# Kernel optimization log

Measured on AMD Instinct MI355X. Metric: run time of the kernel, lower is better.

## Reference

```python
import jax, jax.numpy as jnp
import numpy as np

H = 16  # num_heads

def setup_inputs() -> dict:
    key = jax.random.key(0)
    k1, k2, k3 = jax.random.split(key, 3)
    D = 1024
    x = jax.random.normal(k1, (4, 2048, D), dtype=jnp.float32)
    W_qkv = jax.random.normal(k2, (D, 3 * D), dtype=jnp.float32) * (1.0 / np.sqrt(D))
    b_qkv = jnp.zeros((3 * D,), dtype=jnp.float32)
    W_out = jax.random.normal(k3, (D, D), dtype=jnp.float32) * (1.0 / np.sqrt(D))
    b_out = jnp.zeros((D,), dtype=jnp.float32)
    return {"x": x, "W_qkv": W_qkv, "b_qkv": b_qkv, "W_out": W_out, "b_out": b_out}

def reference(x, W_qkv, b_qkv, W_out, b_out):
    B, S, D = x.shape
    hd = D // H  # head_dim
    qkv = x @ W_qkv + b_qkv  # [B,S,3D]
    q, k, v = jnp.split(qkv, 3, axis=-1)
    # [B,S,D] -> [B,H,S,hd]
    q = q.reshape(B, S, H, hd).transpose(0, 2, 1, 3)
    k = k.reshape(B, S, H, hd).transpose(0, 2, 1, 3)
    v = v.reshape(B, S, H, hd).transpose(0, 2, 1, 3)
    scores = jnp.einsum('bhqd,bhkd->bhqk', q, k) / jnp.sqrt(jnp.float32(hd))
    weights = jax.nn.softmax(scores, axis=-1)  # dropout p=0.0 (eval)
    out = jnp.einsum('bhqk,bhkd->bhqd', weights, v)
    out = out.transpose(0, 2, 1, 3).reshape(B, S, D)
    return out @ W_out + b_out
```

## Files before the change

### kernel.cpp

```cpp
#include <hip/hip_runtime.h>

typedef __bf16 bf16;
typedef __bf16 bf16x4 __attribute__((ext_vector_type(4)));
typedef __bf16 bf16x8 __attribute__((ext_vector_type(8)));
typedef short s16x4 __attribute__((ext_vector_type(4)));
typedef float f32x4 __attribute__((ext_vector_type(4)));

static constexpr int NB = 4;
static constexpr int NS = 2048;
static constexpr int ND = 1024;
static constexpr int NH = 16;
static constexpr int HD = 64;
static constexpr float QSCALE = 0.18033688011112042f;

#define GL16(g, l)                                                             \
    __builtin_amdgcn_global_load_lds(                                          \
        (const __attribute__((address_space(1))) void*)(g),                    \
        (__attribute__((address_space(3))) void*)(l), 16, 0, 0)

static __device__ __forceinline__ unsigned pk2(float a, float b) {
    union { __bf16 h[2]; unsigned u; } t;
    t.h[0] = (__bf16)a; t.h[1] = (__bf16)b;
    return t.u;
}

__global__ void k_conv(const float* __restrict__ in, bf16* __restrict__ out, int n) {
    int i = (blockIdx.x * blockDim.x + threadIdx.x) * 4;
    if (i < n) {
        float4 v = *reinterpret_cast<const float4*>(in + i);
        bf16* o = out + i;
        o[0] = (bf16)v.x; o[1] = (bf16)v.y; o[2] = (bf16)v.z; o[3] = (bf16)v.w;
    }
}

__global__ void k_transconv(const float* __restrict__ in, bf16* __restrict__ out,
                            int K, int N) {
    __shared__ float tile[64][33];
    int k0 = blockIdx.y * 64, n0 = blockIdx.x * 32;
    int tx = threadIdx.x, ty = threadIdx.y;
#pragma unroll
    for (int i = 0; i < 8; ++i)
        tile[ty + 8 * i][tx] = in[(long)(k0 + ty + 8 * i) * N + n0 + tx];
    __syncthreads();
    int t = ty * 32 + tx;
    int row = t >> 3;
    int col8 = (t & 7) * 8;
    bf16x8 v;
#pragma unroll
    for (int c = 0; c < 8; ++c) v[c] = (bf16)tile[col8 + c][row];
    *reinterpret_cast<bf16x8*>(&out[(long)(n0 + row) * K + k0 + col8]) = v;
}

template <int MODE>
__global__ __launch_bounds__(256, 2) void k_gemm(
    const bf16* __restrict__ A, const bf16* __restrict__ Bt,
    const float* __restrict__ bias,
    void* __restrict__ out0, void* __restrict__ out1,
    int M, int Kd)
{
    constexpr int BM = 128, BN = 128, BK = 64;
    __shared__ __align__(16) bf16 As[2][BM * BK];
    __shared__ __align__(16) bf16 Bs[2][BN * BK];

    const int t = threadIdx.x;
    const int wid = t >> 6, lane = t & 63;
    const int wm = wid >> 1, wn = wid & 1;
    const int m0 = blockIdx.y * BM, n0 = blockIdx.x * BN;
    const int lrow = lane & 15, lhi = lane >> 4;

    const int srow0 = wid * 32 + (lane >> 3);
    const int scol = ((lane & 7) ^ (lane >> 3)) * 8;
    const bf16* ag = A + (long)(m0 + srow0) * Kd + scol;
    const bf16* bg = Bt + (long)(n0 + srow0) * Kd + scol;

    auto STAGE = [&](int buf_, int k0_) {
#pragma unroll
        for (int c = 0; c < 4; ++c) {
            GL16(ag + (long)(c * 8) * Kd + k0_, &As[buf_][(wid * 32 + c * 8) * BK]);
            GL16(bg + (long)(c * 8) * Kd + k0_, &Bs[buf_][(wid * 32 + c * 8) * BK]);
        }
    };

    f32x4 acc[4][4] = {};
    const int nt = Kd >> 6;
    const int swzr = (lrow & 7) << 4;
    int co[2];
#pragma unroll
    for (int kk = 0; kk < 2; ++kk)
        co[kk] = ((kk * 64 + lhi * 16) ^ swzr) >> 1;

    STAGE(0, 0);
    int cur = 0;
    for (int tix = 0; tix < nt; ++tix) {
        if (tix + 1 < nt) {
            STAGE(cur ^ 1, (tix + 1) * BK);
            asm volatile("s_waitcnt vmcnt(8)" ::: "memory");
        } else {
            asm volatile("s_waitcnt vmcnt(0)" ::: "memory");
        }
        __builtin_amdgcn_s_barrier();
        __builtin_amdgcn_sched_barrier(0);

        bf16x8 af[2][4], bfr[2][4];
#pragma unroll
        for (int kk = 0; kk < 2; ++kk)
#pragma unroll
            for (int i = 0; i < 4; ++i) {
                af[kk][i]  = *reinterpret_cast<const bf16x8*>(
                    &As[cur][(wm * 64 + i * 16 + lrow) * BK + co[kk]]);
                bfr[kk][i] = *reinterpret_cast<const bf16x8*>(
                    &Bs[cur][(wn * 64 + i * 16 + lrow) * BK + co[kk]]);
            }
        __builtin_amdgcn_s_setprio(1);
#pragma unroll
        for (int kk = 0; kk < 2; ++kk)
#pragma unroll
            for (int i = 0; i < 4; ++i)
#pragma unroll
                for (int j = 0; j < 4; ++j) {
                    if (MODE == 1)
                        acc[i][j] = __builtin_amdgcn_mfma_f32_16x16x32_bf16(
                            af[kk][i], bfr[kk][j], acc[i][j], 0, 0, 0);
                    else
                        acc[i][j] = __builtin_amdgcn_mfma_f32_16x16x32_bf16(
                            bfr[kk][j], af[kk][i], acc[i][j], 0, 0, 0);
                }
        __builtin_amdgcn_s_setprio(0);
        __builtin_amdgcn_s_barrier();
        cur ^= 1;
    }

    const int colbase = n0 + wn * 64;

    if (MODE == 0) {
        bf16* eb = (bf16*)As + wid * 4096;
        const bool isQ = (colbase >> 10) == 0;
#pragma unroll
        for (int j = 0; j < 4; ++j) {
            f32x4 bv = *reinterpret_cast<const f32x4*>(&bias[colbase + j * 16 + 4 * lhi]);
#pragma unroll
            for (int i = 0; i < 4; ++i) {
                int srt = i * 16 + lrow;
                bf16x4 pk;
#pragma unroll
                for (int r = 0; r < 4; ++r) {
                    float v = acc[i][j][r] + bv[r];
                    pk[r] = (bf16)(isQ ? v * QSCALE : v);
                }
                *reinterpret_cast<bf16x4*>(
                    reinterpret_cast<char*>(eb) + srt * 128 +
                    (((j * 16 + 4 * lhi) * 2) ^ ((srt & 7) << 4))) = pk;
            }
        }
        const int h = (colbase & 1023) >> 6;
        bf16* Ob = isQ ? (bf16*)out0 : (bf16*)out1;
#pragma unroll
        for (int it = 0; it < 8; ++it) {
            int rt = it * 8 + (lane >> 3);
            bf16x8 v = *reinterpret_cast<const bf16x8*>(
                reinterpret_cast<char*>(eb) + rt * 128 +
                (((lane & 7) * 16) ^ ((rt & 7) << 4)));
            int row = m0 + wm * 64 + rt;
            int bb = row >> 11, s = row & 2047;
            long bh = (long)bb * NH + h;
            *reinterpret_cast<bf16x8*>(&Ob[(bh * NS + s) * HD + (lane & 7) * 8]) = v;
        }
    } else if (MODE == 1) {
        bf16* eb = (bf16*)As + wid * 4096;
#pragma unroll
        for (int j = 0; j < 4; ++j) {
            float bv = bias[colbase + j * 16 + lrow];
            int drt = j * 16 + lrow;
#pragma unroll
            for (int i = 0; i < 4; ++i) {
                bf16x4 pk;
#pragma unroll
                for (int r = 0; r < 4; ++r) pk[r] = (bf16)(acc[i][j][r] + bv);
                *reinterpret_cast<bf16x4*>(
                    reinterpret_cast<char*>(eb) + drt * 128 +
                    (((i * 16 + 4 * lhi) * 2) ^ ((drt & 7) << 4))) = pk;
            }
        }
        const int h = (colbase & 1023) >> 6;
        const int mrow = m0 + wm * 64;
        const int bb = mrow >> 11, s0 = mrow & 2047;
        bf16* Vt = (bf16*)out0;
        const int pos0 = (lane & 7) * 8;
        const int k0p = (pos0 >> 5) * 32 + ((pos0 >> 3) & 3) * 4;
#pragma unroll
        for (int it = 0; it < 8; ++it) {
            int dt = it * 8 + (lane >> 3);
            int swz = (dt & 7) << 4;
            bf16x4 a = *reinterpret_cast<const bf16x4*>(
                reinterpret_cast<char*>(eb) + dt * 128 + ((2 * k0p) ^ swz));
            bf16x4 b = *reinterpret_cast<const bf16x4*>(
                reinterpret_cast<char*>(eb) + dt * 128 + ((2 * (k0p + 16)) ^ swz));
            bf16x8 v;
#pragma unroll
            for (int r = 0; r < 4; ++r) { v[r] = a[r]; v[4 + r] = b[r]; }
            long bh = (long)bb * NH + h;
            *reinterpret_cast<bf16x8*>(&Vt[(bh * HD + dt) * NS + s0 + pos0]) = v;
        }
    } else {
        float* ef = (float*)As + wid * 2048;
        float* O = (float*)out0;
#pragma unroll
        for (int half = 0; half < 2; ++half) {
#pragma unroll
            for (int i2 = 0; i2 < 2; ++i2) {
                int i = half * 2 + i2;
                int srt = i2 * 16 + lrow;
#pragma unroll
                for (int j = 0; j < 4; ++j) {
                    f32x4 bv = *reinterpret_cast<const f32x4*>(
                        &bias[colbase + j * 16 + 4 * lhi]);
                    f32x4 v = acc[i][j] + bv;
                    *reinterpret_cast<f32x4*>(
                        reinterpret_cast<char*>(ef) + srt * 256 +
                        (((j * 16 + 4 * lhi) * 4) ^ ((srt & 7) << 4))) = v;
                }
            }
#pragma unroll
            for (int it = 0; it < 8; ++it) {
                int rt = it * 4 + (lane >> 4);
                f32x4 v = *reinterpret_cast<const f32x4*>(
                    reinterpret_cast<char*>(ef) + rt * 256 +
                    (((lane & 15) * 16) ^ ((rt & 7) << 4)));
                int row = m0 + wm * 64 + half * 32 + rt;
                *reinterpret_cast<f32x4*>(
                    &O[(long)row * 1024 + colbase + (lane & 15) * 4]) = v;
            }
            asm volatile("" ::: "memory");
        }
    }
}

__global__ __launch_bounds__(512, 4) void k_attn(
    const bf16* __restrict__ Qb, const bf16* __restrict__ Kb,
    const bf16* __restrict__ Vt, bf16* __restrict__ Ao)
{
    constexpr int KB = 64;
    constexpr int NT = NS / KB;
    __shared__ __align__(16) bf16 Ks[2][KB * HD];
    __shared__ __align__(16) bf16 Vs[2][HD * KB];

    const int t = threadIdx.x;
    const int wid = t >> 6, lane = t & 63;
    const int lrow = lane & 15, lhi = lane >> 4;

    const int flat = blockIdx.y * gridDim.x + blockIdx.x;
    const int n = (flat & 7) * 64 + (flat >> 3);
    const int bh = n >> 3;
    const int qw = (n & 7) * 256 + wid * 32;

    const bf16* Qg = Qb + ((long)bh * NS + qw) * HD;
    const bf16* Kg = Kb + (long)bh * NS * HD;
    const bf16* Vg = Vt + (long)bh * HD * NS;

    bf16x8 qf[2][2];
#pragma unroll
    for (int qfr = 0; qfr < 2; ++qfr)
#pragma unroll
        for (int c = 0; c < 2; ++c)
            qf[qfr][c] = *reinterpret_cast<const bf16x8*>(
                Qg + (long)(qfr * 16 + lrow) * HD + c * 32 + lhi * 8);

    f32x4 of[2][4] = {};
    float lsum[2] = {0.f, 0.f};

    const int gsr = lane >> 3;
    const int gsc = ((lane & 7) ^ gsr) * 8;
    const int rb = wid * 8;
    auto STAGE = [&](int buf, int kb) {
        GL16(Kg + (long)(kb + rb + gsr) * HD + gsc, &Ks[buf][rb * 64]);
        GL16(Vg + (long)(rb + gsr) * NS + kb + gsc, &Vs[buf][rb * 64]);
    };

    const int rsw = (lrow & 7) << 4;

    auto COMPUTE = [&](int b_) {
        f32x4 st[2][4] = {};
        __builtin_amdgcn_s_setprio(1);
#pragma unroll
        for (int j = 0; j < 4; ++j)
#pragma unroll
            for (int c = 0; c < 2; ++c) {
                bf16x8 kf = *reinterpret_cast<const bf16x8*>(
                    &Ks[b_][(j * 16 + lrow) * 64 + (((c * 64 + lhi * 16) ^ rsw) >> 1)]);
#pragma unroll
                for (int qfr = 0; qfr < 2; ++qfr)
                    st[qfr][j] = __builtin_amdgcn_mfma_f32_16x16x32_bf16(
                        kf, qf[qfr][c], st[qfr][j], 0, 0, 0);
            }
        __builtin_amdgcn_s_setprio(0);

        union { unsigned u[2]; s16x4 s; } pj[2][4];
#pragma unroll
        for (int qfr = 0; qfr < 2; ++qfr)
#pragma unroll
            for (int j = 0; j < 4; ++j) {
                float e0 = __builtin_amdgcn_exp2f(st[qfr][j][0]);
                float e1 = __builtin_amdgcn_exp2f(st[qfr][j][1]);
                float e2 = __builtin_amdgcn_exp2f(st[qfr][j][2]);
                float e3 = __builtin_amdgcn_exp2f(st[qfr][j][3]);
                lsum[qfr] += (e0 + e1) + (e2 + e3);
                pj[qfr][j].u[0] = pk2(e0, e1);
                pj[qfr][j].u[1] = pk2(e2, e3);
            }

        __builtin_amdgcn_s_setprio(1);
#pragma unroll
        for (int p = 0; p < 2; ++p)
#pragma unroll
            for (int f = 0; f < 4; ++f) {
                union { bf16x8 v; s16x4 h[2]; } vf;
                vf.v = *reinterpret_cast<const bf16x8*>(
                    &Vs[b_][(f * 16 + lrow) * 64 +
                            (((p * 64 + lhi * 16) ^ rsw) >> 1)]);
#pragma unroll
                for (int qfr = 0; qfr < 2; ++qfr) {
                    of[qfr][f] = __builtin_amdgcn_mfma_f32_16x16x16bf16_1k(
                        vf.h[0], pj[qfr][2 * p].s, of[qfr][f], 0, 0, 0);
                    of[qfr][f] = __builtin_amdgcn_mfma_f32_16x16x16bf16_1k(
                        vf.h[1], pj[qfr][2 * p + 1].s, of[qfr][f], 0, 0, 0);
                }
            }
        __builtin_amdgcn_s_setprio(0);
    };

    STAGE(0, 0);
    int cur = 0;
    for (int it = 0; it < NT; ++it) {
        if (it + 1 < NT) {
            STAGE(cur ^ 1, (it + 1) * KB);
            asm volatile("s_waitcnt vmcnt(2)" ::: "memory");
        } else {
            asm volatile("s_waitcnt vmcnt(0)" ::: "memory");
        }
        __builtin_amdgcn_s_barrier();
        __builtin_amdgcn_sched_barrier(0);
        COMPUTE(cur);
        __builtin_amdgcn_s_barrier();
        cur ^= 1;
    }

#pragma unroll
    for (int qfr = 0; qfr < 2; ++qfr) {
        lsum[qfr] += __shfl_xor(lsum[qfr], 16);
        lsum[qfr] += __shfl_xor(lsum[qfr], 32);
    }

    bf16* eb = (wid < 4) ? ((bf16*)Ks + wid * 2048) : ((bf16*)Vs + (wid - 4) * 2048);
#pragma unroll
    for (int qfr = 0; qfr < 2; ++qfr) {
        float inv = 1.0f / lsum[qfr];
        int srt = qfr * 16 + lrow;
#pragma unroll
        for (int f = 0; f < 4; ++f) {
            bf16x4 pk;
#pragma unroll
            for (int r = 0; r < 4; ++r) pk[r] = (bf16)(of[qfr][f][r] * inv);
            *reinterpret_cast<bf16x4*>(
                reinterpret_cast<char*>(eb) + srt * 128 +
                (((f * 16 + 4 * lhi) * 2) ^ ((srt & 7) << 4))) = pk;
        }
    }
    const int bb = bh >> 4, h = bh & 15;
#pragma unroll
    for (int it = 0; it < 4; ++it) {
        int rt = it * 8 + (lane >> 3);
        bf16x8 v = *reinterpret_cast<const bf16x8*>(
            reinterpret_cast<char*>(eb) + rt * 128 +
            (((lane & 7) * 16) ^ ((rt & 7) << 4)));
        int s = qw + rt;
        *reinterpret_cast<bf16x8*>(
            &Ao[((long)bb * NS + s) * ND + h * HD + (lane & 7) * 8]) = v;
    }
}

extern "C" void kernel_launch(void* const* d_in, const int* in_sizes, int n_in,
                              void* d_out, int out_size, void* d_ws, size_t ws_size,
                              hipStream_t stream) {
    const float* x    = (const float*)d_in[0];
    const float* Wqkv = (const float*)d_in[1];
    const float* bqkv = (const float*)d_in[2];
    const float* Wout = (const float*)d_in[3];
    const float* bout = (const float*)d_in[4];
    float* out = (float*)d_out;

    char* ws = (char*)d_ws;
    bf16* Xb  = (bf16*)(ws);
    bf16* Wqt = (bf16*)(ws + 16777216);
    bf16* Wot = (bf16*)(ws + 23068672);
    bf16* Qb  = (bf16*)(ws + 25165824);
    bf16* Kb  = (bf16*)(ws + 41943040);
    bf16* Vt  = (bf16*)(ws + 58720256);
    bf16* Ab  = (bf16*)(ws + 75497472);

    k_conv<<<dim3(8192), dim3(256), 0, stream>>>(x, Xb, NB * NS * ND);
    k_transconv<<<dim3(96, 16), dim3(32, 8), 0, stream>>>(Wqkv, Wqt, ND, 3 * ND);
    k_transconv<<<dim3(32, 16), dim3(32, 8), 0, stream>>>(Wout, Wot, ND, ND);

    k_gemm<0><<<dim3(16, 64), dim3(256), 0, stream>>>(
        Xb, Wqt, bqkv, Qb, Kb, NB * NS, ND);
    k_gemm<1><<<dim3(8, 64), dim3(256), 0, stream>>>(
        Xb, Wqt + (long)2048 * ND, bqkv + 2048, Vt, nullptr, NB * NS, ND);

    k_attn<<<dim3(8, 64), dim3(512), 0, stream>>>(Qb, Kb, Vt, Ab);

    k_gemm<2><<<dim3(8, 64), dim3(256), 0, stream>>>(
        Ab, Wot, bout, out, nullptr, NB * NS, ND);
}
```

Before: 196.7 us.

## Merge Q/K/V projections into one GEMM launch and double attention key block

Fuses the separate QK and V projection GEMMs into a single kernel over all 3D output columns, with the V tiles transposed through LDS using scalar bf16 gathers. This removes one launch and the second pass that re-read X, and fills the GPU with one larger grid. The attention kernel now stages 128 keys per iteration (two 64-key halves) to halve the barrier and wait count per key, at the cost of more LDS and a scalar-gather epilogue for V.

```diff
diff --git a/kernel.cpp b/kernel.cpp
--- a/kernel.cpp
+++ b/kernel.cpp
@@ -51,12 +51,11 @@
     *reinterpret_cast<bf16x8*>(&out[(long)(n0 + row) * K + k0 + col8]) = v;
 }
 
-template <int MODE>
-__global__ __launch_bounds__(256, 2) void k_gemm(
+__global__ __launch_bounds__(256, 2) void k_gemmQKV(
     const bf16* __restrict__ A, const bf16* __restrict__ Bt,
     const float* __restrict__ bias,
-    void* __restrict__ out0, void* __restrict__ out1,
-    int M, int Kd)
+    bf16* __restrict__ Qb, bf16* __restrict__ Kb, bf16* __restrict__ Vt,
+    int Kd)
 {
     constexpr int BM = 128, BN = 128, BK = 64;
     __shared__ __align__(16) bf16 As[2][BM * BK];
@@ -117,121 +116,172 @@
 #pragma unroll
             for (int i = 0; i < 4; ++i)
 #pragma unroll
-                for (int j = 0; j < 4; ++j) {
-                    if (MODE == 1)
-                        acc[i][j] = __builtin_amdgcn_mfma_f32_16x16x32_bf16(
-                            af[kk][i], bfr[kk][j], acc[i][j], 0, 0, 0);
-                    else
-                        acc[i][j] = __builtin_amdgcn_mfma_f32_16x16x32_bf16(
-                            bfr[kk][j], af[kk][i], acc[i][j], 0, 0, 0);
-                }
+                for (int j = 0; j < 4; ++j)
+                    acc[i][j] = __builtin_amdgcn_mfma_f32_16x16x32_bf16(
+                        bfr[kk][j], af[kk][i], acc[i][j], 0, 0, 0);
         __builtin_amdgcn_s_setprio(0);
         __builtin_amdgcn_s_barrier();
         cur ^= 1;
     }
 
     const int colbase = n0 + wn * 64;
-
-    if (MODE == 0) {
-        bf16* eb = (bf16*)As + wid * 4096;
-        const bool isQ = (colbase >> 10) == 0;
-#pragma unroll
-        for (int j = 0; j < 4; ++j) {
-            f32x4 bv = *reinterpret_cast<const f32x4*>(&bias[colbase + j * 16 + 4 * lhi]);
-#pragma unroll
-            for (int i = 0; i < 4; ++i) {
-                int srt = i * 16 + lrow;
-                bf16x4 pk;
-#pragma unroll
-                for (int r = 0; r < 4; ++r) {
-                    float v = acc[i][j][r] + bv[r];
-                    pk[r] = (bf16)(isQ ? v * QSCALE : v);
-                }
-                *reinterpret_cast<bf16x4*>(
-                    reinterpret_cast<char*>(eb) + srt * 128 +
-                    (((j * 16 + 4 * lhi) * 2) ^ ((srt & 7) << 4))) = pk;
-            }
-        }
-        const int h = (colbase & 1023) >> 6;
-        bf16* Ob = isQ ? (bf16*)out0 : (bf16*)out1;
+    const int which = colbase >> 10;
+    const bool isQ = (which == 0);
+
+    bf16* eb = (bf16*)As + wid * 4096;
+#pragma unroll
+    for (int j = 0; j < 4; ++j) {
+        f32x4 bv = *reinterpret_cast<const f32x4*>(&bias[colbase + j * 16 + 4 * lhi]);
+#pragma unroll
+        for (int i = 0; i < 4; ++i) {
+            int srt = i * 16 + lrow;
+            bf16x4 pk;
+#pragma unroll
+            for (int r = 0; r < 4; ++r) {
+                float v = acc[i][j][r] + bv[r];
+                pk[r] = (bf16)(isQ ? v * QSCALE : v);
+            }
+            *reinterpret_cast<bf16x4*>(
+                reinterpret_cast<char*>(eb) + srt * 128 +
+                (((j * 16 + 4 * lhi) * 2) ^ ((srt & 7) << 4))) = pk;
+        }
+    }
+    const int h = (colbase & 1023) >> 6;
+    const int mrow = m0 + wm * 64;
+    const int bb = mrow >> 11, s0 = mrow & 2047;
+    const long bh = (long)bb * NH + h;
+
+    if (which < 2) {
+        bf16* Ob = isQ ? Qb : Kb;
 #pragma unroll
         for (int it = 0; it < 8; ++it) {
             int rt = it * 8 + (lane >> 3);
             bf16x8 v = *reinterpret_cast<const bf16x8*>(
                 reinterpret_cast<char*>(eb) + rt * 128 +
                 (((lane & 7) * 16) ^ ((rt & 7) << 4)));
-            int row = m0 + wm * 64 + rt;
-            int bb = row >> 11, s = row & 2047;
-            long bh = (long)bb * NH + h;
+            int s = s0 + rt;
             *reinterpret_cast<bf16x8*>(&Ob[(bh * NS + s) * HD + (lane & 7) * 8]) = v;
         }
-    } else if (MODE == 1) {
-        bf16* eb = (bf16*)As + wid * 4096;
-#pragma unroll
-        for (int j = 0; j < 4; ++j) {
-            float bv = bias[colbase + j * 16 + lrow];
-            int drt = j * 16 + lrow;
-#pragma unroll
-            for (int i = 0; i < 4; ++i) {
-                bf16x4 pk;
-#pragma unroll
-                for (int r = 0; r < 4; ++r) pk[r] = (bf16)(acc[i][j][r] + bv);
-                *reinterpret_cast<bf16x4*>(
-                    reinterpret_cast<char*>(eb) + drt * 128 +
-                    (((i * 16 + 4 * lhi) * 2) ^ ((drt & 7) << 4))) = pk;
-            }
-        }
-        const int h = (colbase & 1023) >> 6;
-        const int mrow = m0 + wm * 64;
-        const int bb = mrow >> 11, s0 = mrow & 2047;
-        bf16* Vt = (bf16*)out0;
+    } else {
+        const int p = (lane & 7) >> 2;
+        const int l4 = (lane & 3) * 4;
         const int pos0 = (lane & 7) * 8;
-        const int k0p = (pos0 >> 5) * 32 + ((pos0 >> 3) & 3) * 4;
 #pragma unroll
         for (int it = 0; it < 8; ++it) {
             int dt = it * 8 + (lane >> 3);
-            int swz = (dt & 7) << 4;
-            bf16x4 a = *reinterpret_cast<const bf16x4*>(
-                reinterpret_cast<char*>(eb) + dt * 128 + ((2 * k0p) ^ swz));
-            bf16x4 b = *reinterpret_cast<const bf16x4*>(
-                reinterpret_cast<char*>(eb) + dt * 128 + ((2 * (k0p + 16)) ^ swz));
             bf16x8 v;
 #pragma unroll
-            for (int r = 0; r < 4; ++r) { v[r] = a[r]; v[4 + r] = b[r]; }
-            long bh = (long)bb * NH + h;
+            for (int j = 0; j < 8; ++j) {
+                int k = 32 * p + 16 * (j >> 2) + l4 + (j & 3);
+                v[j] = *reinterpret_cast<const bf16*>(
+                    reinterpret_cast<char*>(eb) + k * 128 +
+                    ((dt * 2) ^ ((k & 7) << 4)));
+            }
             *reinterpret_cast<bf16x8*>(&Vt[(bh * HD + dt) * NS + s0 + pos0]) = v;
         }
-    } else {
-        float* ef = (float*)As + wid * 2048;
-        float* O = (float*)out0;
-#pragma unroll
-        for (int half = 0; half < 2; ++half) {
-#pragma unroll
-            for (int i2 = 0; i2 < 2; ++i2) {
-                int i = half * 2 + i2;
-                int srt = i2 * 16 + lrow;
-#pragma unroll
-                for (int j = 0; j < 4; ++j) {
-                    f32x4 bv = *reinterpret_cast<const f32x4*>(
-                        &bias[colbase + j * 16 + 4 * lhi]);
-                    f32x4 v = acc[i][j] + bv;
-                    *reinterpret_cast<f32x4*>(
-                        reinterpret_cast<char*>(ef) + srt * 256 +
-                        (((j * 16 + 4 * lhi) * 4) ^ ((srt & 7) << 4))) = v;
-                }
-            }
-#pragma unroll
-            for (int it = 0; it < 8; ++it) {
-                int rt = it * 4 + (lane >> 4);
-                f32x4 v = *reinterpret_cast<const f32x4*>(
-                    reinterpret_cast<char*>(ef) + rt * 256 +
-                    (((lane & 15) * 16) ^ ((rt & 7) << 4)));
-                int row = m0 + wm * 64 + half * 32 + rt;
+    }
+}
+
+__global__ __launch_bounds__(256, 2) void k_gemmO(
+    const bf16* __restrict__ A, const bf16* __restrict__ Bt,
+    const float* __restrict__ bias, float* __restrict__ O, int Kd)
+{
+    constexpr int BM = 128, BN = 128, BK = 64;
+    __shared__ __align__(16) bf16 As[2][BM * BK];
+    __shared__ __align__(16) bf16 Bs[2][BN * BK];
+
+    const int t = threadIdx.x;
+    const int wid = t >> 6, lane = t & 63;
+    const int wm = wid >> 1, wn = wid & 1;
+    const int m0 = blockIdx.y * BM, n0 = blockIdx.x * BN;
+    const int lrow = lane & 15, lhi = lane >> 4;
+
+    const int srow0 = wid * 32 + (lane >> 3);
+    const int scol = ((lane & 7) ^ (lane >> 3)) * 8;
+    const bf16* ag = A + (long)(m0 + srow0) * Kd + scol;
+    const bf16* bg = Bt + (long)(n0 + srow0) * Kd + scol;
+
+    auto STAGE = [&](int buf_, int k0_) {
+#pragma unroll
+        for (int c = 0; c < 4; ++c) {
+            GL16(ag + (long)(c * 8) * Kd + k0_, &As[buf_][(wid * 32 + c * 8) * BK]);
+            GL16(bg + (long)(c * 8) * Kd + k0_, &Bs[buf_][(wid * 32 + c * 8) * BK]);
+        }
+    };
+
+    f32x4 acc[4][4] = {};
+    const int nt = Kd >> 6;
+    const int swzr = (lrow & 7) << 4;
+    int co[2];
+#pragma unroll
+    for (int kk = 0; kk < 2; ++kk)
+        co[kk] = ((kk * 64 + lhi * 16) ^ swzr) >> 1;
+
+    STAGE(0, 0);
+    int cur = 0;
+    for (int tix = 0; tix < nt; ++tix) {
+        if (tix + 1 < nt) {
+            STAGE(cur ^ 1, (tix + 1) * BK);
+            asm volatile("s_waitcnt vmcnt(8)" ::: "memory");
+        } else {
+            asm volatile("s_waitcnt vmcnt(0)" ::: "memory");
+        }
+        __builtin_amdgcn_s_barrier();
+        __builtin_amdgcn_sched_barrier(0);
+
+        bf16x8 af[2][4], bfr[2][4];
+#pragma unroll
+        for (int kk = 0; kk < 2; ++kk)
+#pragma unroll
+            for (int i = 0; i < 4; ++i) {
+                af[kk][i]  = *reinterpret_cast<const bf16x8*>(
+                    &As[cur][(wm * 64 + i * 16 + lrow) * BK + co[kk]]);
+                bfr[kk][i] = *reinterpret_cast<const bf16x8*>(
+                    &Bs[cur][(wn * 64 + i * 16 + lrow) * BK + co[kk]]);
+            }
+        __builtin_amdgcn_s_setprio(1);
+#pragma unroll
+        for (int kk = 0; kk < 2; ++kk)
+#pragma unroll
+            for (int i = 0; i < 4; ++i)
+#pragma unroll
+                for (int j = 0; j < 4; ++j)
+                    acc[i][j] = __builtin_amdgcn_mfma_f32_16x16x32_bf16(
+                        bfr[kk][j], af[kk][i], acc[i][j], 0, 0, 0);
+        __builtin_amdgcn_s_setprio(0);
+        __builtin_amdgcn_s_barrier();
+        cur ^= 1;
+    }
+
+    const int colbase = n0 + wn * 64;
+    float* ef = (float*)As + wid * 2048;
+#pragma unroll
+    for (int half = 0; half < 2; ++half) {
+#pragma unroll
+        for (int i2 = 0; i2 < 2; ++i2) {
+            int i = half * 2 + i2;
+            int srt = i2 * 16 + lrow;
+#pragma unroll
+            for (int j = 0; j < 4; ++j) {
+                f32x4 bv = *reinterpret_cast<const f32x4*>(
+                    &bias[colbase + j * 16 + 4 * lhi]);
+                f32x4 v = acc[i][j] + bv;
                 *reinterpret_cast<f32x4*>(
-                    &O[(long)row * 1024 + colbase + (lane & 15) * 4]) = v;
-            }
-            asm volatile("" ::: "memory");
-        }
+                    reinterpret_cast<char*>(ef) + srt * 256 +
+                    (((j * 16 + 4 * lhi) * 4) ^ ((srt & 7) << 4))) = v;
+            }
+        }
+#pragma unroll
+        for (int it = 0; it < 8; ++it) {
+            int rt = it * 4 + (lane >> 4);
+            f32x4 v = *reinterpret_cast<const f32x4*>(
+                reinterpret_cast<char*>(ef) + rt * 256 +
+                (((lane & 15) * 16) ^ ((rt & 7) << 4)));
+            int row = m0 + wm * 64 + half * 32 + rt;
+            *reinterpret_cast<f32x4*>(
+                &O[(long)row * 1024 + colbase + (lane & 15) * 4]) = v;
+        }
+        asm volatile("" ::: "memory");
     }
 }
 
@@ -239,10 +289,10 @@
     const bf16* __restrict__ Qb, const bf16* __restrict__ Kb,
     const bf16* __restrict__ Vt, bf16* __restrict__ Ao)
 {
-    constexpr int KB = 64;
+    constexpr int KB = 128;
     constexpr int NT = NS / KB;
     __shared__ __align__(16) bf16 Ks[2][KB * HD];
-    __shared__ __align__(16) bf16 Vs[2][HD * KB];
+    __shared__ __align__(16) bf16 Vs[2][2][64 * 64];
 
     const int t = threadIdx.x;
     const int wid = t >> 6, lane = t & 63;
@@ -270,15 +320,16 @@
 
     const int gsr = lane >> 3;
     const int gsc = ((lane & 7) ^ gsr) * 8;
-    const int rb = wid * 8;
     auto STAGE = [&](int buf, int kb) {
-        GL16(Kg + (long)(kb + rb + gsr) * HD + gsc, &Ks[buf][rb * 64]);
-        GL16(Vg + (long)(rb + gsr) * NS + kb + gsc, &Vs[buf][rb * 64]);
+        GL16(Kg + (long)(kb + wid * 16 + gsr) * HD + gsc,     &Ks[buf][(wid * 16) * 64]);
+        GL16(Kg + (long)(kb + wid * 16 + 8 + gsr) * HD + gsc, &Ks[buf][(wid * 16 + 8) * 64]);
+        GL16(Vg + (long)(wid * 8 + gsr) * NS + kb + gsc,      &Vs[buf][0][(wid * 8) * 64]);
+        GL16(Vg + (long)(wid * 8 + gsr) * NS + kb + 64 + gsc, &Vs[buf][1][(wid * 8) * 64]);
     };
 
     const int rsw = (lrow & 7) << 4;
 
-    auto COMPUTE = [&](int b_) {
+    auto COMPUTE = [&](int b_, int ho) {
         f32x4 st[2][4] = {};
         __builtin_amdgcn_s_setprio(1);
 #pragma unroll
@@ -286,7 +337,8 @@
 #pragma unroll
             for (int c = 0; c < 2; ++c) {
                 bf16x8 kf = *reinterpret_cast<const bf16x8*>(
-                    &Ks[b_][(j * 16 + lrow) * 64 + (((c * 64 + lhi * 16) ^ rsw) >> 1)]);
+                    &Ks[b_][(ho * 64 + j * 16 + lrow) * 64 +
+                            (((c * 64 + lhi * 16) ^ rsw) >> 1)]);
 #pragma unroll
                 for (int qfr = 0; qfr < 2; ++qfr)
                     st[qfr][j] = __builtin_amdgcn_mfma_f32_16x16x32_bf16(
@@ -315,8 +367,8 @@
             for (int f = 0; f < 4; ++f) {
                 union { bf16x8 v; s16x4 h[2]; } vf;
                 vf.v = *reinterpret_cast<const bf16x8*>(
-                    &Vs[b_][(f * 16 + lrow) * 64 +
-                            (((p * 64 + lhi * 16) ^ rsw) >> 1)]);
+                    &Vs[b_][ho][(f * 16 + lrow) * 64 +
+                                (((p * 64 + lhi * 16) ^ rsw) >> 1)]);
 #pragma unroll
                 for (int qfr = 0; qfr < 2; ++qfr) {
                     of[qfr][f] = __builtin_amdgcn_mfma_f32_16x16x16bf16_1k(
@@ -333,13 +385,14 @@
     for (int it = 0; it < NT; ++it) {
         if (it + 1 < NT) {
             STAGE(cur ^ 1, (it + 1) * KB);
-            asm volatile("s_waitcnt vmcnt(2)" ::: "memory");
+            asm volatile("s_waitcnt vmcnt(4)" ::: "memory");
         } else {
             asm volatile("s_waitcnt vmcnt(0)" ::: "memory");
         }
         __builtin_amdgcn_s_barrier();
         __builtin_amdgcn_sched_barrier(0);
-        COMPUTE(cur);
+        COMPUTE(cur, 0);
+        COMPUTE(cur, 1);
         __builtin_amdgcn_s_barrier();
         cur ^= 1;
     }
@@ -350,7 +403,8 @@
         lsum[qfr] += __shfl_xor(lsum[qfr], 32);
     }
 
-    bf16* eb = (wid < 4) ? ((bf16*)Ks + wid * 2048) : ((bf16*)Vs + (wid - 4) * 2048);
+    bf16* eb = (wid < 4) ? ((bf16*)Ks + wid * 2048)
+                         : ((bf16*)Vs + (wid - 4) * 2048);
 #pragma unroll
     for (int qfr = 0; qfr < 2; ++qfr) {
         float inv = 1.0f / lsum[qfr];
@@ -401,13 +455,11 @@
     k_transconv<<<dim3(96, 16), dim3(32, 8), 0, stream>>>(Wqkv, Wqt, ND, 3 * ND);
     k_transconv<<<dim3(32, 16), dim3(32, 8), 0, stream>>>(Wout, Wot, ND, ND);
 
-    k_gemm<0><<<dim3(16, 64), dim3(256), 0, stream>>>(
-        Xb, Wqt, bqkv, Qb, Kb, NB * NS, ND);
-    k_gemm<1><<<dim3(8, 64), dim3(256), 0, stream>>>(
-        Xb, Wqt + (long)2048 * ND, bqkv + 2048, Vt, nullptr, NB * NS, ND);
+    k_gemmQKV<<<dim3(24, 64), dim3(256), 0, stream>>>(
+        Xb, Wqt, bqkv, Qb, Kb, Vt, ND);
 
     k_attn<<<dim3(8, 64), dim3(512), 0, stream>>>(Qb, Kb, Vt, Ab);
 
-    k_gemm<2><<<dim3(8, 64), dim3(256), 0, stream>>>(
-        Ab, Wot, bout, out, nullptr, NB * NS, ND);
-}
+    k_gemmO<<<dim3(8, 64), dim3(256), 0, stream>>>(
+        Ab, Wot, bout, out, ND);
+}
```

Result: slower. 392.5 us (+99.6%).
